# Performance work log

Measured on AMD Instinct MI355X. Metric: run time of the kernel, lower is better.

Reference implementation:

```python
import jax, jax.numpy as jnp
import numpy as np

N_NODES = 100000
N_EDGES = 1600000
IN_CH = 128
OUT_CH = 128

def setup_inputs() -> dict:
    key = jax.random.key(0)
    k1, k2, k3, k4, k5 = jax.random.split(key, 5)
    x = jax.random.normal(k1, (N_NODES, IN_CH), dtype=jnp.float32)
    src = jax.random.randint(k2, (N_EDGES,), 0, N_NODES, dtype=jnp.int64)
    dst = jax.random.randint(k3, (N_EDGES,), 0, N_NODES, dtype=jnp.int64)
    edge_index = jnp.stack([src, dst], axis=0)
    W = jax.random.normal(k4, (OUT_CH, IN_CH), dtype=jnp.float32) * (1.0 / np.sqrt(IN_CH))
    b = jax.random.normal(k5, (OUT_CH,), dtype=jnp.float32) * 0.01
    return {"x": x, "edge_index": edge_index, "W": W, "b": b}

def reference(x, edge_index, W, b):
    n = x.shape[0]
    src, dst = edge_index[0], edge_index[1]
    loop = jnp.arange(n, dtype=edge_index.dtype)
    src_all = jnp.concatenate([src, loop])  # [E+N]
    dst_all = jnp.concatenate([dst, loop])  # [E+N]
    # in-degree (with self loops) per node
    deg = jax.ops.segment_sum(jnp.ones_like(dst_all, dtype=x.dtype), dst_all, num_segments=n)
    norm = (deg[src_all] * deg[dst_all]) ** -0.5
    norm = jnp.where(jnp.isinf(norm), 0.0, norm)
    h = x @ W.T + b  # [N, out_ch]
    msg = h[src_all] * norm[:, None]  # [E+N, out_ch]
    out = jax.ops.segment_sum(msg, dst_all, num_segments=n)  # [N, out_ch]
    return out
```

## Files before the change

kernel.cpp:

```cpp
#include <hip/hip_runtime.h>
#include <hip/hip_bf16.h>


#define N_NODES 100000
#define N_EDGES 1600000
#define CH 128
#define NC 49
#define CAPC 34816
#define NCHUNK 17
#define NFB 1563
#define FCAP 1280

__device__ inline unsigned short f2bf(float f) {
    unsigned u = __float_as_uint(f);
    u += 0x7fffu + ((u >> 16) & 1u);
    return (unsigned short)(u >> 16);
}
__device__ inline float bflo(unsigned u) { return __uint_as_float(u << 16); }
__device__ inline float bfhi(unsigned u) { return __uint_as_float(u & 0xffff0000u); }

__global__ __launch_bounds__(256) void k_sortA(const int* __restrict__ src,
                                               const int* __restrict__ dst,
                                               int* __restrict__ ctail,
                                               unsigned* __restrict__ E1) {
    __shared__ int hist[NC];
    __shared__ int boff[NC + 1];
    __shared__ int cur[NC];
    __shared__ int gb[NC];
    __shared__ unsigned stage[2048];
    const int t    = threadIdx.x;
    const int base = blockIdx.x * 2048;
    const int n    = min(2048, N_EDGES - base);

    if (t < NC) hist[t] = 0;
    __syncthreads();

    int s[8], d[8];
#pragma unroll
    for (int h = 0; h < 2; ++h) {
        int idx = h * 1024 + 4 * t;
        if (idx < n) {
            int4 sv = *(const int4*)&src[base + idx];
            int4 dv = *(const int4*)&dst[base + idx];
            s[4*h+0] = sv.x; s[4*h+1] = sv.y; s[4*h+2] = sv.z; s[4*h+3] = sv.w;
            d[4*h+0] = dv.x; d[4*h+1] = dv.y; d[4*h+2] = dv.z; d[4*h+3] = dv.w;
        } else {
            d[4*h+0] = d[4*h+1] = d[4*h+2] = d[4*h+3] = -1;
            s[4*h+0] = s[4*h+1] = s[4*h+2] = s[4*h+3] = 0;
        }
    }
#pragma unroll
    for (int j = 0; j < 8; ++j)
        if (d[j] >= 0) atomicAdd(&hist[d[j] >> 11], 1);
    __syncthreads();

    if (t < NC) gb[t] = atomicAdd(&ctail[t], hist[t]);
    if (t == 0) {
        int run = 0;
        for (int k = 0; k < NC; ++k) { boff[k] = run; run += hist[k]; }
        boff[NC] = run;
    }
    __syncthreads();
    if (t < NC) cur[t] = boff[t];
    __syncthreads();

#pragma unroll
    for (int j = 0; j < 8; ++j)
        if (d[j] >= 0) {
            int k = d[j] >> 11;
            int pos = atomicAdd(&cur[k], 1);
            stage[pos] = ((unsigned)s[j] << 11) | (unsigned)(d[j] & 2047);
        }
    __syncthreads();

    const int tot = boff[NC];
    for (int i = t; i < tot; i += 256) {
        int lo = 0, hi = NC;
#pragma unroll
        for (int it = 0; it < 6; ++it) {
            int mid = (lo + hi) >> 1;
            bool c = (boff[mid] <= i);
            lo = c ? mid : lo;
            hi = c ? hi : mid;
        }
        int p = gb[lo] + (i - boff[lo]);
        if (p < CAPC) E1[(size_t)lo * CAPC + p] = stage[i];
    }
}

__global__ __launch_bounds__(256) void k_sortB(const unsigned* __restrict__ E1,
                                               const int* __restrict__ ctail,
                                               int* __restrict__ ftail,
                                               unsigned* __restrict__ E2) {
    __shared__ int hist[32];
    __shared__ int boff[33];
    __shared__ int cur[32];
    __shared__ int gb[32];
    __shared__ unsigned stage[2048];
    const int cb = blockIdx.x / NCHUNK;
    const int ch = blockIdx.x % NCHUNK;
    const int t  = threadIdx.x;
    int cnt = ctail[cb]; if (cnt > CAPC) cnt = CAPC;
    const int begin = ch * 2048;
    int n = cnt - begin;
    if (n <= 0) return;
    if (n > 2048) n = 2048;
    const unsigned* e1 = E1 + (size_t)cb * CAPC + begin;

    if (t < 32) hist[t] = 0;
    __syncthreads();

    for (int i = t; i < n; i += 256)
        atomicAdd(&hist[(e1[i] >> 6) & 31], 1);
    __syncthreads();

    if (t < 32) gb[t] = atomicAdd(&ftail[cb * 32 + t], hist[t]);
    if (t == 0) {
        int run = 0;
        for (int k = 0; k < 32; ++k) { boff[k] = run; run += hist[k]; }
        boff[32] = run;
    }
    __syncthreads();
    if (t < 32) cur[t] = boff[t];
    __syncthreads();

    for (int i = t; i < n; i += 256) {
        unsigned v = e1[i];
        int k = (v >> 6) & 31;
        int pos = atomicAdd(&cur[k], 1);
        stage[pos] = ((v >> 11) << 6) | (v & 63);
    }
    __syncthreads();

    const int tot = boff[32];
    for (int i = t; i < tot; i += 256) {
        int lo = 0, hi = 32;
#pragma unroll
        for (int it = 0; it < 5; ++it) {
            int mid = (lo + hi) >> 1;
            bool c = (boff[mid] <= i);
            lo = c ? mid : lo;
            hi = c ? hi : mid;
        }
        int p = gb[lo] + (i - boff[lo]);
        int fb = cb * 32 + lo;
        if (p < FCAP) E2[(size_t)fb * FCAP + p] = stage[i];
    }
}

__global__ __launch_bounds__(256) void k_deg(const unsigned* __restrict__ E2,
                                             const int* __restrict__ ftail,
                                             float* __restrict__ rinv) {
    __shared__ int bins[64];
    const int fb = blockIdx.x;
    const int t  = threadIdx.x;
    if (t < 64) bins[t] = 0;
    int n = ftail[fb]; if (n > FCAP) n = FCAP;
    __syncthreads();
    const unsigned* e2 = E2 + (size_t)fb * FCAP;
    for (int i = t; i < n; i += 256) atomicAdd(&bins[e2[i] & 63], 1);
    __syncthreads();
    if (t < 64) {
        int node = fb * 64 + t;
        if (node < N_NODES) rinv[node] = rsqrtf((float)(bins[t] + 1));
    }
}

__global__ __launch_bounds__(256) void k_gemm(const float* __restrict__ x,
                                              const float* __restrict__ W,
                                              const float* __restrict__ b,
                                              const float* __restrict__ rinv,
                                              unsigned short* __restrict__ hs) {
    __shared__ __align__(16) float xs[32][36];
    __shared__ __align__(16) float ws[32][132];
    const int t  = threadIdx.x;
    const int tx = t & 31;
    const int ty = t >> 5;
    const int row0 = blockIdx.x * 32;

    float acc[4][4] = {};

    for (int k0 = 0; k0 < CH; k0 += 32) {
        {
            int r  = t >> 5;
            int kk = t & 31;
            for (int p = 0; p < 4; ++p) {
                int rr = r + p * 8;
                xs[rr][kk] = x[(size_t)(row0 + rr) * CH + k0 + kk];
            }
            int o = t >> 5;
            for (int p = 0; p < 16; ++p) {
                int oo = o + p * 8;
                ws[kk][oo] = W[(size_t)oo * CH + k0 + kk];
            }
        }
        __syncthreads();

        for (int k4 = 0; k4 < 32; k4 += 4) {
            float4 xv[4], wv[4];
            for (int i = 0; i < 4; ++i)
                xv[i] = *(const float4*)&xs[ty + 8 * i][k4];
            for (int j = 0; j < 4; ++j)
                wv[j] = *(const float4*)&ws[k4 + j][4 * tx];
            for (int i = 0; i < 4; ++i) {
                acc[i][0] += xv[i].x * wv[0].x; acc[i][1] += xv[i].x * wv[0].y;
                acc[i][2] += xv[i].x * wv[0].z; acc[i][3] += xv[i].x * wv[0].w;
                acc[i][0] += xv[i].y * wv[1].x; acc[i][1] += xv[i].y * wv[1].y;
                acc[i][2] += xv[i].y * wv[1].z; acc[i][3] += xv[i].y * wv[1].w;
                acc[i][0] += xv[i].z * wv[2].x; acc[i][1] += xv[i].z * wv[2].y;
                acc[i][2] += xv[i].z * wv[2].z; acc[i][3] += xv[i].z * wv[2].w;
                acc[i][0] += xv[i].w * wv[3].x; acc[i][1] += xv[i].w * wv[3].y;
                acc[i][2] += xv[i].w * wv[3].z; acc[i][3] += xv[i].w * wv[3].w;
            }
        }
        __syncthreads();
    }

    float4 bv = *(const float4*)&b[4 * tx];
    for (int i = 0; i < 4; ++i) {
        int r = row0 + ty + 8 * i;
        float ri = rinv[r];
        ushort4 o4;
        o4.x = f2bf(ri * (acc[i][0] + bv.x));
        o4.y = f2bf(ri * (acc[i][1] + bv.y));
        o4.z = f2bf(ri * (acc[i][2] + bv.z));
        o4.w = f2bf(ri * (acc[i][3] + bv.w));
        *(ushort4*)&hs[(size_t)r * CH + 4 * tx] = o4;
    }
}

#define ACC8(u)                                                            \
    do {                                                                   \
        acc[0] += bflo((u).x); acc[1] += bfhi((u).x);                      \
        acc[2] += bflo((u).y); acc[3] += bfhi((u).y);                      \
        acc[4] += bflo((u).z); acc[5] += bfhi((u).z);                      \
        acc[6] += bflo((u).w); acc[7] += bfhi((u).w);                      \
    } while (0)

__global__ __launch_bounds__(256) void k_spmm(const unsigned* __restrict__ E2,
                                              const int* __restrict__ ftail,
                                              const float* __restrict__ rinv,
                                              const unsigned short* __restrict__ hs,
                                              float* __restrict__ out) {
    __shared__ int bins[64];
    __shared__ int boff[65];
    __shared__ int cur[64];
    __shared__ int srt[FCAP];
    const int fb    = blockIdx.x;
    const int node0 = fb * 64;
    const int t     = threadIdx.x;
    const unsigned* e2 = E2 + (size_t)fb * FCAP;
    const uint4* hp = (const uint4*)hs;

    if (t < 64) bins[t] = 0;
    int n = ftail[fb]; if (n > FCAP) n = FCAP;
    __syncthreads();

    for (int i = t; i < n; i += 256) atomicAdd(&bins[e2[i] & 63], 1);
    __syncthreads();

    if (t == 0) {
        int run = 0;
        for (int k = 0; k < 64; ++k) { boff[k] = run; run += bins[k]; }
        boff[64] = run;
    }
    __syncthreads();
    if (t < 64) cur[t] = boff[t];
    __syncthreads();

    for (int i = t; i < n; i += 256) {
        unsigned v = e2[i];
        int pos = atomicAdd(&cur[v & 63], 1);
        srt[pos] = (int)(v >> 6);
    }
    __syncthreads();

    const int grp  = t >> 4;
    const int lane = t & 15;
#pragma unroll
    for (int r = 0; r < 4; ++r) {
        const int nl   = grp * 4 + r;
        const int node = node0 + nl;
        if (node >= N_NODES) continue;
        float acc[8] = {};
        {
            uint4 u = hp[(size_t)node * 16 + lane];
            ACC8(u);
        }
        int e  = boff[nl];
        int e1 = boff[nl + 1];
        for (; e + 4 <= e1; e += 4) {
            int s0 = srt[e + 0];
            int s1 = srt[e + 1];
            int s2 = srt[e + 2];
            int s3 = srt[e + 3];
            uint4 u0 = hp[(size_t)s0 * 16 + lane];
            uint4 u1 = hp[(size_t)s1 * 16 + lane];
            uint4 u2 = hp[(size_t)s2 * 16 + lane];
            uint4 u3 = hp[(size_t)s3 * 16 + lane];
            ACC8(u0); ACC8(u1); ACC8(u2); ACC8(u3);
        }
        for (; e < e1; ++e) {
            uint4 u = hp[(size_t)srt[e] * 16 + lane];
            ACC8(u);
        }
        float ri = rinv[node];
        float4 o0, o1;
        o0.x = ri * acc[0]; o0.y = ri * acc[1]; o0.z = ri * acc[2]; o0.w = ri * acc[3];
        o1.x = ri * acc[4]; o1.y = ri * acc[5]; o1.z = ri * acc[6]; o1.w = ri * acc[7];
        *(float4*)&out[(size_t)node * CH + lane * 8]     = o0;
        *(float4*)&out[(size_t)node * CH + lane * 8 + 4] = o1;
    }
}

extern "C" void kernel_launch(void* const* d_in, const int* in_sizes, int n_in,
                              void* d_out, int out_size, void* d_ws, size_t ws_size,
                              hipStream_t stream) {
    const float* x  = (const float*)d_in[0];
    const int*   ei = (const int*)d_in[1];
    const float* W  = (const float*)d_in[2];
    const float* b  = (const float*)d_in[3];
    float* out = (float*)d_out;

    const int* src = ei;
    const int* dst = ei + N_EDGES;

    int*      ctail = (int*)d_ws;
    int*      ftail = ctail + 64;
    float*    rinv  = (float*)(ftail + 1600);
    unsigned* E1    = (unsigned*)(rinv + N_NODES);
    unsigned* E2    = E1 + (size_t)NC * CAPC;
    unsigned short* hs = (unsigned short*)(E2 + (size_t)NFB * FCAP);

    hipMemsetAsync(ctail, 0, (64 + 1600) * sizeof(int), stream);

    k_sortA<<<(N_EDGES + 2047) / 2048, 256, 0, stream>>>(src, dst, ctail, E1);
    k_sortB<<<NC * NCHUNK, 256, 0, stream>>>(E1, ctail, ftail, E2);
    k_deg<<<NFB, 256, 0, stream>>>(E2, ftail, rinv);
    k_gemm<<<N_NODES / 32, 256, 0, stream>>>(x, W, b, rinv, hs);
    k_spmm<<<NFB, 256, 0, stream>>>(E2, ftail, rinv, hs, out);
}
```

Measured before the change: 252.6 us.

## Use split-bf16 MFMA for the dense transform and deepen SpMM gather unroll

Rewrites the x·Wᵀ GEMM to use bf16 MFMA instructions with a hi/lo split of both operands (three products) to keep near-fp32 accuracy. W is converted once per block into swizzled LDS, and each wave computes 32 rows by 128 columns. The SpMM adds an 8-way gather unroll for more loads in flight and switches output writes to nontemporal stores. The split costs three MFMAs per tile plus conversion work, and the GEMM epilogue now writes scalar bf16 values with strided stores.

```diff
diff --git a/kernel.cpp b/kernel.cpp
--- a/kernel.cpp
+++ b/kernel.cpp
@@ -10,6 +10,9 @@
 #define NCHUNK 17
 #define NFB 1563
 #define FCAP 1280
+
+using bf16x8 = __attribute__((ext_vector_type(8))) short;
+using f32x4  = __attribute__((ext_vector_type(4))) float;
 
 __device__ inline unsigned short f2bf(float f) {
     unsigned u = __float_as_uint(f);
@@ -166,66 +169,106 @@
     }
 }
 
+__device__ inline void cvt8(const float4 a, const float4 b, bf16x8& h, bf16x8& l) {
+    bf16x8 H, L;
+#define CV(i, f) { unsigned short hb = f2bf(f); H[i] = (short)hb;               \
+                   L[i] = (short)f2bf((f) - __uint_as_float((unsigned)hb << 16)); }
+    CV(0, a.x) CV(1, a.y) CV(2, a.z) CV(3, a.w)
+    CV(4, b.x) CV(5, b.y) CV(6, b.z) CV(7, b.w)
+#undef CV
+    h = H; l = L;
+}
+
+#define MFMA(a, b, c) __builtin_amdgcn_mfma_f32_16x16x32_bf16((a), (b), (c), 0, 0, 0)
+
 __global__ __launch_bounds__(256) void k_gemm(const float* __restrict__ x,
                                               const float* __restrict__ W,
                                               const float* __restrict__ b,
                                               const float* __restrict__ rinv,
                                               unsigned short* __restrict__ hs) {
-    __shared__ __align__(16) float xs[32][36];
-    __shared__ __align__(16) float ws[32][132];
-    const int t  = threadIdx.x;
-    const int tx = t & 31;
-    const int ty = t >> 5;
-    const int row0 = blockIdx.x * 32;
-
-    float acc[4][4] = {};
-
-    for (int k0 = 0; k0 < CH; k0 += 32) {
-        {
-            int r  = t >> 5;
-            int kk = t & 31;
-            for (int p = 0; p < 4; ++p) {
-                int rr = r + p * 8;
-                xs[rr][kk] = x[(size_t)(row0 + rr) * CH + k0 + kk];
-            }
-            int o = t >> 5;
-            for (int p = 0; p < 16; ++p) {
-                int oo = o + p * 8;
-                ws[kk][oo] = W[(size_t)oo * CH + k0 + kk];
-            }
-        }
-        __syncthreads();
-
-        for (int k4 = 0; k4 < 32; k4 += 4) {
-            float4 xv[4], wv[4];
-            for (int i = 0; i < 4; ++i)
-                xv[i] = *(const float4*)&xs[ty + 8 * i][k4];
-            for (int j = 0; j < 4; ++j)
-                wv[j] = *(const float4*)&ws[k4 + j][4 * tx];
-            for (int i = 0; i < 4; ++i) {
-                acc[i][0] += xv[i].x * wv[0].x; acc[i][1] += xv[i].x * wv[0].y;
-                acc[i][2] += xv[i].x * wv[0].z; acc[i][3] += xv[i].x * wv[0].w;
-                acc[i][0] += xv[i].y * wv[1].x; acc[i][1] += xv[i].y * wv[1].y;
-                acc[i][2] += xv[i].y * wv[1].z; acc[i][3] += xv[i].y * wv[1].w;
-                acc[i][0] += xv[i].z * wv[2].x; acc[i][1] += xv[i].z * wv[2].y;
-                acc[i][2] += xv[i].z * wv[2].z; acc[i][3] += xv[i].z * wv[2].w;
-                acc[i][0] += xv[i].w * wv[3].x; acc[i][1] += xv[i].w * wv[3].y;
-                acc[i][2] += xv[i].w * wv[3].z; acc[i][3] += xv[i].w * wv[3].w;
-            }
-        }
-        __syncthreads();
-    }
-
-    float4 bv = *(const float4*)&b[4 * tx];
-    for (int i = 0; i < 4; ++i) {
-        int r = row0 + ty + 8 * i;
-        float ri = rinv[r];
-        ushort4 o4;
-        o4.x = f2bf(ri * (acc[i][0] + bv.x));
-        o4.y = f2bf(ri * (acc[i][1] + bv.y));
-        o4.z = f2bf(ri * (acc[i][2] + bv.z));
-        o4.w = f2bf(ri * (acc[i][3] + bv.w));
-        *(ushort4*)&hs[(size_t)r * CH + 4 * tx] = o4;
+    __shared__ __align__(16) unsigned short wh[CH * CH];
+    __shared__ __align__(16) unsigned short wl[CH * CH];
+    const int t = threadIdx.x;
+
+    for (int c = t; c < 2048; c += 256) {
+        int o   = c >> 4;
+        int kk  = (c & 15) << 3;
+        const float* wp = &W[(size_t)o * CH + kk];
+        float4 w0 = *(const float4*)wp;
+        float4 w1 = *(const float4*)(wp + 4);
+        bf16x8 H, L;
+        cvt8(w0, w1, H, L);
+        unsigned boff = ((unsigned)((o << 8) | (kk << 1))) ^ ((unsigned)(o & 7) << 4);
+        *(bf16x8*)((char*)wh + boff) = H;
+        *(bf16x8*)((char*)wl + boff) = L;
+    }
+    __syncthreads();
+
+    const int lane = t & 63;
+    const int l15  = lane & 15;
+    const int lhi  = lane >> 4;
+    const int kc   = lhi << 3;
+    const int row_base = blockIdx.x * 128 + (t >> 6) * 32;
+
+    int r0 = row_base + l15;       if (r0 > N_NODES - 1) r0 = N_NODES - 1;
+    int r1 = row_base + 16 + l15;  if (r1 > N_NODES - 1) r1 = N_NODES - 1;
+    const float* x0 = &x[(size_t)r0 * CH + kc];
+    const float* x1 = &x[(size_t)r1 * CH + kc];
+
+    float4 xa[4][2], xb[4][2];
+#pragma unroll
+    for (int ks = 0; ks < 4; ++ks) {
+        xa[ks][0] = *(const float4*)(x0 + ks * 32);
+        xa[ks][1] = *(const float4*)(x0 + ks * 32 + 4);
+        xb[ks][0] = *(const float4*)(x1 + ks * 32);
+        xb[ks][1] = *(const float4*)(x1 + ks * 32 + 4);
+    }
+
+    f32x4 acc[2][8];
+#pragma unroll
+    for (int rf = 0; rf < 2; ++rf)
+#pragma unroll
+        for (int cf = 0; cf < 8; ++cf)
+            acc[rf][cf] = (f32x4){0.f, 0.f, 0.f, 0.f};
+
+#pragma unroll
+    for (int ks = 0; ks < 4; ++ks) {
+        bf16x8 ah0, al0, ah1, al1;
+        cvt8(xa[ks][0], xa[ks][1], ah0, al0);
+        cvt8(xb[ks][0], xb[ks][1], ah1, al1);
+        const unsigned kb = (unsigned)((ks * 32 + kc) << 1);
+#pragma unroll
+        for (int cf = 0; cf < 8; ++cf) {
+            int o = cf * 16 + l15;
+            unsigned boff = (((unsigned)(o << 8)) + kb) ^ ((unsigned)(o & 7) << 4);
+            bf16x8 bh = *(const bf16x8*)((const char*)wh + boff);
+            bf16x8 bl = *(const bf16x8*)((const char*)wl + boff);
+            acc[0][cf] = MFMA(ah0, bh, acc[0][cf]);
+            acc[1][cf] = MFMA(ah1, bh, acc[1][cf]);
+            acc[0][cf] = MFMA(al0, bh, acc[0][cf]);
+            acc[1][cf] = MFMA(al1, bh, acc[1][cf]);
+            acc[0][cf] = MFMA(ah0, bl, acc[0][cf]);
+            acc[1][cf] = MFMA(ah1, bl, acc[1][cf]);
+        }
+    }
+
+    float bcol[8];
+#pragma unroll
+    for (int cf = 0; cf < 8; ++cf) bcol[cf] = b[cf * 16 + l15];
+
+#pragma unroll
+    for (int rf = 0; rf < 2; ++rf) {
+        int rb = row_base + rf * 16 + lhi * 4;
+        if (rb >= N_NODES) continue;
+        float4 ri4 = *(const float4*)&rinv[rb];
+        float ri[4] = {ri4.x, ri4.y, ri4.z, ri4.w};
+#pragma unroll
+        for (int j = 0; j < 4; ++j) {
+            size_t ro = (size_t)(rb + j) * CH;
+#pragma unroll
+            for (int cf = 0; cf < 8; ++cf)
+                hs[ro + cf * 16 + l15] = f2bf(ri[j] * (acc[rf][cf][j] + bcol[cf]));
+        }
     }
 }
 
@@ -289,6 +332,20 @@
         }
         int e  = boff[nl];
         int e1 = boff[nl + 1];
+        for (; e + 8 <= e1; e += 8) {
+            int s0 = srt[e + 0], s1 = srt[e + 1], s2 = srt[e + 2], s3 = srt[e + 3];
+            int s4 = srt[e + 4], s5 = srt[e + 5], s6 = srt[e + 6], s7 = srt[e + 7];
+            uint4 u0 = hp[(size_t)s0 * 16 + lane];
+            uint4 u1 = hp[(size_t)s1 * 16 + lane];
+            uint4 u2 = hp[(size_t)s2 * 16 + lane];
+            uint4 u3 = hp[(size_t)s3 * 16 + lane];
+            uint4 u4 = hp[(size_t)s4 * 16 + lane];
+            uint4 u5 = hp[(size_t)s5 * 16 + lane];
+            uint4 u6 = hp[(size_t)s6 * 16 + lane];
+            uint4 u7 = hp[(size_t)s7 * 16 + lane];
+            ACC8(u0); ACC8(u1); ACC8(u2); ACC8(u3);
+            ACC8(u4); ACC8(u5); ACC8(u6); ACC8(u7);
+        }
         for (; e + 4 <= e1; e += 4) {
             int s0 = srt[e + 0];
             int s1 = srt[e + 1];
@@ -305,11 +362,11 @@
             ACC8(u);
         }
         float ri = rinv[node];
-        float4 o0, o1;
-        o0.x = ri * acc[0]; o0.y = ri * acc[1]; o0.z = ri * acc[2]; o0.w = ri * acc[3];
-        o1.x = ri * acc[4]; o1.y = ri * acc[5]; o1.z = ri * acc[6]; o1.w = ri * acc[7];
-        *(float4*)&out[(size_t)node * CH + lane * 8]     = o0;
-        *(float4*)&out[(size_t)node * CH + lane * 8 + 4] = o1;
+        f32x4 o0, o1;
+        o0[0] = ri * acc[0]; o0[1] = ri * acc[1]; o0[2] = ri * acc[2]; o0[3] = ri * acc[3];
+        o1[0] = ri * acc[4]; o1[1] = ri * acc[5]; o1[2] = ri * acc[6]; o1[3] = ri * acc[7];
+        __builtin_nontemporal_store(o0, (f32x4*)&out[(size_t)node * CH + lane * 8]);
+        __builtin_nontemporal_store(o1, (f32x4*)&out[(size_t)node * CH + lane * 8 + 4]);
     }
 }
 
@@ -337,6 +394,6 @@
     k_sortA<<<(N_EDGES + 2047) / 2048, 256, 0, stream>>>(src, dst, ctail, E1);
     k_sortB<<<NC * NCHUNK, 256, 0, stream>>>(E1, ctail, ftail, E2);
     k_deg<<<NFB, 256, 0, stream>>>(E2, ftail, rinv);
-    k_gemm<<<N_NODES / 32, 256, 0, stream>>>(x, W, b, rinv, hs);
+    k_gemm<<<(N_NODES + 127) / 128, 256, 0, stream>>>(x, W, b, rinv, hs);
     k_spmm<<<NFB, 256, 0, stream>>>(E2, ftail, rinv, hs, out);
 }
```

After: 231.9 us. 1.09x faster.
